# Performance work log

Measured on AMD Instinct MI355X. Metric: run time of the kernel, lower is better.

The kernel has to match this reference:

```python
import jax, jax.numpy as jnp
import numpy as np

DIM = 256
NUM_HEADS = 4
HEAD_DIM = DIM // NUM_HEADS
SCALE = HEAD_DIM ** -0.5


def setup_inputs() -> dict:
    key = jax.random.key(0)
    ks = jax.random.split(key, 6)
    B, S = 4, 4096
    x = jax.random.normal(ks[0], (B, S, DIM), dtype=jnp.float32)
    # nn.Linear weights are [out, in]; we store them that way and apply x @ W.T
    wq = jax.random.normal(ks[1], (DIM, DIM), dtype=jnp.float32) * (DIM ** -0.5)
    wk = jax.random.normal(ks[2], (DIM, DIM), dtype=jnp.float32) * (DIM ** -0.5)
    wv = jax.random.normal(ks[3], (DIM, DIM), dtype=jnp.float32) * (DIM ** -0.5)
    wo = jax.random.normal(ks[4], (DIM, DIM), dtype=jnp.float32) * (DIM ** -0.5)
    bo = jax.random.normal(ks[5], (DIM,), dtype=jnp.float32) * 0.02
    return {"x": x, "wq": wq, "wk": wk, "wv": wv, "wo": wo, "bo": bo}


def reference(x, wq, wk, wv, wo, bo):
    B, S, D = x.shape
    H, Hd = NUM_HEADS, HEAD_DIM
    # project and split heads: [B, H, S, Hd]
    q = (x @ wq.T).reshape(B, S, H, Hd).transpose(0, 2, 1, 3)
    k = (x @ wk.T).reshape(B, S, H, Hd).transpose(0, 2, 1, 3)
    v = (x @ wv.T).reshape(B, S, H, Hd).transpose(0, 2, 1, 3)
    attn = jnp.einsum('bhqd,bhkd->bhqk', q, k) * SCALE
    attn = jax.nn.softmax(attn, axis=-1)  # dropout is identity in eval mode
    out = jnp.einsum('bhqk,bhkd->bhqd', attn, v)
    out = out.transpose(0, 2, 1, 3).reshape(B, S, D)
    return out @ wo.T + bo
```

## Files before the change

### kernel.cpp

```cpp
#include <hip/hip_runtime.h>
#include <hip/hip_bf16.h>
#include <stdint.h>

#define DIM    256
#define NH     4
#define HD     64
#define BATCH  4
#define SEQ    4096
#define NTOK   (BATCH*SEQ)

typedef __bf16    bf16_t;
typedef _Float16  f16_t;
typedef _Float16  f16x8  __attribute__((ext_vector_type(8)));
typedef _Float16  f16x4  __attribute__((ext_vector_type(4)));
typedef float     f32x4  __attribute__((ext_vector_type(4)));
typedef float     f32x16 __attribute__((ext_vector_type(16)));
typedef unsigned short u16x8 __attribute__((ext_vector_type(8)));
typedef unsigned int   u32;
typedef u32 u32x2 __attribute__((ext_vector_type(2)));
typedef u32 u32x4 __attribute__((ext_vector_type(4)));

#define MFMA_F16    __builtin_amdgcn_mfma_f32_16x16x32_f16
#define MFMA32_F16  __builtin_amdgcn_mfma_f32_32x32x16_f16

#define QSCALE 0.18033688011112042f

#define WS_XA    ((size_t)0)
#define WS_Q     ((size_t)4194304)
#define WS_K     ((size_t)8388608)
#define WS_VT    ((size_t)12582912)
#define WS_W     ((size_t)16777216)
#define WS_BO    ((size_t)17039360)
#define WS_OATT  WS_XA

__device__ __forceinline__ size_t tiled_idx(int row, int k) {
  return ((size_t)(row >> 4) * 32 + (k >> 3)) * 128 + (row & 15) * 8 + (k & 7);
}

__device__ __forceinline__ void glds16(const void* g, void* l) {
  __builtin_amdgcn_global_load_lds(
      (const __attribute__((address_space(1))) void*)g,
      (__attribute__((address_space(3))) void*)l, 16, 0, 0);
}

__device__ __forceinline__ int detect_mode(const uint32_t* wq_u32) {
  uint32_t word = wq_u32[(threadIdx.x & 63) * 431 + 17];
  uint32_t b = (word >> 8) & 0x7fu;
  unsigned long long m = __ballot(b >= 0x38u && b <= 0x3fu);
  return (__popcll(m) >= 32) ? 0 : 1;
}

__device__ __forceinline__ f16x8 cvt_chunk(const void* src, size_t elem, int mode) {
  f16x8 r;
  if (mode) {
    const float* s = (const float*)src + elem;
    #pragma unroll
    for (int j = 0; j < 8; ++j) r[j] = (f16_t)s[j];
  } else {
    u16x8 v = *(const u16x8*)((const unsigned short*)src + elem);
    #pragma unroll
    for (int j = 0; j < 8; ++j) r[j] = (f16_t)__uint_as_float(((unsigned)v[j]) << 16);
  }
  return r;
}

__device__ __forceinline__ u32 pkh(float a, float b) {
  auto h = __builtin_amdgcn_cvt_pkrtz(a, b);
  return __builtin_bit_cast(u32, h);
}

__device__ __forceinline__ void swap32(u32& x, u32& y) {
#if __has_builtin(__builtin_amdgcn_permlane32_swap)
  u32x2 r = __builtin_amdgcn_permlane32_swap(x, y, false, false);
  x = r[0]; y = r[1];
#else
  u32 xp = __shfl_xor((int)x, 32), yp = __shfl_xor((int)y, 32);
  const bool h = (threadIdx.x & 32) != 0;
  u32 nx = h ? yp : x;
  u32 ny = h ? y  : xp;
  x = nx; y = ny;
#endif
}

__global__ __launch_bounds__(256) void cvt_all_kernel(
    const void* __restrict__ x,
    const void* __restrict__ wq, const void* __restrict__ wk,
    const void* __restrict__ wv, const void* __restrict__ wo,
    const void* __restrict__ bo,
    f16_t* __restrict__ xA, f16_t* __restrict__ wT,
    float* __restrict__ bof) {
  __shared__ int s_mode;
  if (threadIdx.x < 64) {
    int m = detect_mode((const uint32_t*)wq);
    if (threadIdx.x == 0) s_mode = m;
  }
  __syncthreads();
  const int mode = s_mode;
  const int bid = blockIdx.x;

  if (bid < 2048) {
    int idx = bid * 256 + (int)threadIdx.x;
    int tok = idx >> 5, kc = idx & 31;
    f16x8 r = cvt_chunk(x, (size_t)tok * DIM + kc * 8, mode);
    *(f16x8*)(xA + tiled_idx(tok, kc * 8)) = r;
  } else if (bid < 2176) {
    int idx = (bid - 2048) * 256 + (int)threadIdx.x;
    int which = idx >> 13, local = idx & 8191;
    const void* src = (which == 0) ? wq : (which == 1) ? wk : (which == 2) ? wv : wo;
    int n = local >> 5, kc = local & 31;
    f16x8 r = cvt_chunk(src, (size_t)n * DIM + kc * 8, mode);
    *(f16x8*)(wT + (size_t)which * 65536 + tiled_idx(n, kc * 8)) = r;
  } else {
    int i = threadIdx.x;
    bof[i] = mode ? ((const float*)bo)[i] : (float)((const bf16_t*)bo)[i];
  }
}

__global__ __launch_bounds__(256) void proj_fused_kernel(
    const f16_t* __restrict__ xA, const f16_t* __restrict__ wT,
    f16_t* __restrict__ q, f16_t* __restrict__ kk, f16_t* __restrict__ vt) {
  const int z    = blockIdx.z;
  const f16_t* w = wT + (size_t)z * 65536;
  const int lane = threadIdx.x & 63;
  const int wvi  = threadIdx.x >> 6;
  const int c    = lane & 15;
  const int g    = lane >> 4;

  if (z < 2) {
    const float scale = (z == 0) ? QSCALE : 1.0f;
    const int m0 = blockIdx.x * 64 + wvi * 16;
    const int n0 = blockIdx.y * 64;
    const f16_t* abase = xA + (size_t)(m0 >> 4) * 4096 + c * 8;
    const f16_t* bbase = w + (size_t)(n0 >> 4) * 4096 + c * 8;
    f32x4 acc[4] = {};
    #pragma unroll
    for (int ks = 0; ks < 8; ++ks) {
      const int kc = (ks * 4 + g) * 128;
      f16x8 a = *(const f16x8*)(abase + kc);
      #pragma unroll
      for (int nt = 0; nt < 4; ++nt) {
        f16x8 b = *(const f16x8*)(bbase + (size_t)nt * 4096 + kc);
        acc[nt] = MFMA_F16(a, b, acc[nt], 0, 0, 0);
      }
    }
    if (z == 0) {
      #pragma unroll
      for (int nt = 0; nt < 4; ++nt) {
        const int n = n0 + nt * 16 + c;
        const int h = n >> 6, d = n & 63;
        #pragma unroll
        for (int r = 0; r < 4; ++r) {
          const int tok = m0 + g * 4 + r;
          const int b = tok >> 12, s = tok & 4095;
          q[(size_t)((b * NH + h) * SEQ + s) * HD + d] = (f16_t)(acc[nt][r] * scale);
        }
      }
    } else {
      #pragma unroll
      for (int nt = 0; nt < 4; ++nt) {
        const int n = n0 + nt * 16 + c;
        const int h = n >> 6, d = n & 63;
        #pragma unroll
        for (int r = 0; r < 4; ++r) {
          const int tok = m0 + g * 4 + r;
          const int b = tok >> 12, s = tok & 4095;
          const int kt = s >> 6, row = s & 63;
          const int ch = (d >> 3) ^ (row & 7);
          kk[(size_t)(b * NH + h) * (SEQ * HD) + kt * 4096 + row * 64 + ch * 8 + (d & 7)]
              = (f16_t)acc[nt][r];
        }
      }
    }
  } else {
    const int m0 = blockIdx.y * 64 + wvi * 16;
    const int n0 = blockIdx.x * 64;
    const f16_t* abase = w + (size_t)(m0 >> 4) * 4096 + c * 8;
    const f16_t* bbase = xA + (size_t)(n0 >> 4) * 4096 + c * 8;
    f32x4 acc[4] = {};
    #pragma unroll
    for (int ks = 0; ks < 8; ++ks) {
      const int kc = (ks * 4 + g) * 128;
      f16x8 a = *(const f16x8*)(abase + kc);
      #pragma unroll
      for (int nt = 0; nt < 4; ++nt) {
        f16x8 b = *(const f16x8*)(bbase + (size_t)nt * 4096 + kc);
        acc[nt] = MFMA_F16(a, b, acc[nt], 0, 0, 0);
      }
    }
    #pragma unroll
    for (int nt = 0; nt < 4; ++nt) {
      const int tok = n0 + nt * 16 + c;
      const int b = tok >> 12, s = tok & 4095;
      const int kt = s >> 6, ko = s & 63;
      #pragma unroll
      for (int r = 0; r < 4; ++r) {
        const int vd = m0 + g * 4 + r;
        const int h = vd >> 6, d = vd & 63;
        const int ch = (ko >> 3) ^ (d & 7);
        vt[(size_t)(b * NH + h) * (SEQ * HD) + kt * 4096 + d * 64 + ch * 8 + (ko & 7)]
            = (f16_t)acc[nt][r];
      }
    }
  }
}

__global__ __launch_bounds__(256, 2) void attn_kernel(
    const f16_t* __restrict__ q, const f16_t* __restrict__ kimg,
    const f16_t* __restrict__ vimg, f16_t* __restrict__ o) {
  __shared__ __align__(16) f16_t smem[16896];

  const int tid = threadIdx.x;
  const int l   = tid & 63;
  const int w   = tid >> 6;
  const int wq_ = w & 1;
  const int wk_ = w >> 1;
  const int ql  = l & 31;
  const int hi  = l >> 5;
  const int bh  = blockIdx.x;
  const int q0  = blockIdx.y * 128;

  const f16_t* qb = q + ((size_t)bh * SEQ + q0 + wq_ * 64 + ql) * HD + hi * 8;
  f16x8 qf[2][4];
  #pragma unroll
  for (int qt = 0; qt < 2; ++qt)
    #pragma unroll
    for (int s = 0; s < 4; ++s)
      qf[qt][s] = *(const f16x8*)(qb + (size_t)qt * 32 * HD + s * 16);

  const char* kbase = (const char*)kimg + (size_t)bh * (SEQ * HD * 2);
  const char* vbase = (const char*)vimg + (size_t)bh * (SEQ * HD * 2);
  char* sB = (char*)smem;
  const int t16 = tid * 16;

  const int qx  = ql & 7;
  const int krow = wk_ * 32 + ql;
  int koff[4], voff[2][2];
  #pragma unroll
  for (int s = 0; s < 4; ++s)
    koff[s] = krow * 64 + (((s * 2 + hi) ^ qx) * 8);
  #pragma unroll
  for (int dt = 0; dt < 2; ++dt) {
    const int drow = dt * 32 + ql;
    #pragma unroll
    for (int kb = 0; kb < 2; ++kb)
      voff[dt][kb] = 4096 + drow * 64 + (((wk_ * 4 + kb * 2 + hi) ^ qx) * 8);
  }

  f32x16 acc[2][2] = {};
  float lsum[2] = {0.f, 0.f};

  glds16(kbase + t16,        sB + t16);
  glds16(kbase + 4096 + t16, sB + 4096 + t16);
  glds16(vbase + t16,        sB + 8192 + t16);
  glds16(vbase + 4096 + t16, sB + 12288 + t16);
  __syncthreads();

  for (int kt = 0; kt < SEQ / 64; ++kt) {
    const int bufo = (kt & 1) * 8192;
    const int bufB = (kt & 1) * 16384;
    if (kt < SEQ / 64 - 1) {
      const int nxtB = bufB ^ 16384;
      const size_t go = (size_t)(kt + 1) * 8192;
      glds16(kbase + go + t16,        sB + nxtB + t16);
      glds16(kbase + go + 4096 + t16, sB + nxtB + 4096 + t16);
      glds16(vbase + go + t16,        sB + nxtB + 8192 + t16);
      glds16(vbase + go + 4096 + t16, sB + nxtB + 12288 + t16);
    }

    f16x8 kf[4], vf[2][2];
    #pragma unroll
    for (int s = 0; s < 4; ++s)
      kf[s] = *(const f16x8*)(smem + bufo + koff[s]);
    #pragma unroll
    for (int dt = 0; dt < 2; ++dt)
      #pragma unroll
      for (int kb = 0; kb < 2; ++kb)
        vf[dt][kb] = *(const f16x8*)(smem + bufo + voff[dt][kb]);

    f16x8 pf[2][2];
    #pragma unroll
    for (int qt = 0; qt < 2; ++qt) {
      f32x16 st = {};
      #pragma unroll
      for (int s = 0; s < 4; ++s) st = MFMA32_F16(kf[s], qf[qt][s], st, 0, 0, 0);
      float p[16];
      #pragma unroll
      for (int r = 0; r < 16; ++r) p[r] = __builtin_amdgcn_exp2f(st[r]);
      float ls = 0.f;
      #pragma unroll
      for (int r = 0; r < 16; r += 4) ls += (p[r] + p[r + 1]) + (p[r + 2] + p[r + 3]);
      lsum[qt] += ls;
      #pragma unroll
      for (int kb = 0; kb < 2; ++kb) {
        u32 d0 = pkh(p[kb * 8 + 0], p[kb * 8 + 1]);
        u32 d1 = pkh(p[kb * 8 + 2], p[kb * 8 + 3]);
        u32 d2 = pkh(p[kb * 8 + 4], p[kb * 8 + 5]);
        u32 d3 = pkh(p[kb * 8 + 6], p[kb * 8 + 7]);
        swap32(d0, d2);
        swap32(d1, d3);
        u32x4 fd; fd[0] = d0; fd[1] = d1; fd[2] = d2; fd[3] = d3;
        pf[qt][kb] = __builtin_bit_cast(f16x8, fd);
      }
    }

    #pragma unroll
    for (int dt = 0; dt < 2; ++dt)
      #pragma unroll
      for (int qt = 0; qt < 2; ++qt) {
        f32x16 a = acc[dt][qt];
        a = MFMA32_F16(vf[dt][0], pf[qt][0], a, 0, 0, 0);
        a = MFMA32_F16(vf[dt][1], pf[qt][1], a, 0, 0, 0);
        acc[dt][qt] = a;
      }

    __syncthreads();
  }

  float* lred = (float*)(smem + 16384);
  #pragma unroll
  for (int qt = 0; qt < 2; ++qt) {
    lsum[qt] += __shfl_xor(lsum[qt], 32);
    if (hi == 0) lred[w * 64 + qt * 32 + ql] = lsum[qt];
  }
  float* red = (float*)smem;
  if (wk_ == 1) {
    #pragma unroll
    for (int t = 0; t < 4; ++t) {
      f32x16 a = acc[t >> 1][t & 1];
      #pragma unroll
      for (int qd = 0; qd < 4; ++qd) {
        f32x4 v = { a[qd * 4], a[qd * 4 + 1], a[qd * 4 + 2], a[qd * 4 + 3] };
        *(f32x4*)(red + wq_ * 4096 + (t * 4 + qd) * 256 + l * 4) = v;
      }
    }
  }
  __syncthreads();
  if (wk_ == 0) {
    float inv[2];
    #pragma unroll
    for (int qt = 0; qt < 2; ++qt)
      inv[qt] = 1.0f / (lred[w * 64 + qt * 32 + ql] + lred[(w + 2) * 64 + qt * 32 + ql]);

    const int b = bh >> 2, h = bh & 3;
    #pragma unroll
    for (int dt = 0; dt < 2; ++dt)
      #pragma unroll
      for (int qt = 0; qt < 2; ++qt) {
        const int t = dt * 2 + qt;
        f32x16 a = acc[dt][qt];
        const int tokg = b * SEQ + q0 + wq_ * 64 + qt * 32 + ql;
        const size_t rowbase = (size_t)(tokg >> 4) * 32 * 128 + (tokg & 15) * 8 + hi * 4;
        #pragma unroll
        for (int qd = 0; qd < 4; ++qd) {
          f32x4 v = *(const f32x4*)(red + wq_ * 4096 + (t * 4 + qd) * 256 + l * 4);
          f16x4 ov = { (f16_t)((a[qd * 4 + 0] + v[0]) * inv[qt]),
                       (f16_t)((a[qd * 4 + 1] + v[1]) * inv[qt]),
                       (f16_t)((a[qd * 4 + 2] + v[2]) * inv[qt]),
                       (f16_t)((a[qd * 4 + 3] + v[3]) * inv[qt]) };
          *(f16x4*)(o + rowbase + (size_t)(h * 8 + dt * 4 + qd) * 128) = ov;
        }
      }
  }
}

__global__ __launch_bounds__(256) void out_proj_kernel(
    const f16_t* __restrict__ aA, const f16_t* __restrict__ wT,
    const float* __restrict__ bo, void* __restrict__ outv,
    const void* __restrict__ wq_raw) {
  __shared__ int s_mode;
  if (threadIdx.x < 64) {
    int m = detect_mode((const uint32_t*)wq_raw);
    if (threadIdx.x == 0) s_mode = m;
  }
  __syncthreads();
  const int mode = s_mode;

  const int lane = threadIdx.x & 63;
  const int wv   = threadIdx.x >> 6;
  const int c    = lane & 15;
  const int g    = lane >> 4;
  const int m0   = blockIdx.x * 64 + wv * 16;
  const int n0   = blockIdx.y * 64;

  const f16_t* abase = aA + (size_t)(m0 >> 4) * 4096 + c * 8;
  const f16_t* bbase = wT + (size_t)(n0 >> 4) * 4096 + c * 8;
  f32x4 acc[4] = {};

  #pragma unroll
  for (int ks = 0; ks < 8; ++ks) {
    const int kc = (ks * 4 + g) * 128;
    f16x8 a = *(const f16x8*)(abase + kc);
    #pragma unroll
    for (int nt = 0; nt < 4; ++nt) {
      f16x8 b = *(const f16x8*)(bbase + (size_t)nt * 4096 + kc);
      acc[nt] = MFMA_F16(a, b, acc[nt], 0, 0, 0);
    }
  }

  #pragma unroll
  for (int nt = 0; nt < 4; ++nt) {
    const int n = n0 + nt * 16 + c;
    const float bias = bo[n];
    #pragma unroll
    for (int r = 0; r < 4; ++r) {
      const int tok = m0 + g * 4 + r;
      const float val = acc[nt][r] + bias;
      const size_t idx = (size_t)tok * DIM + n;
      if (mode) ((float*)outv)[idx] = val;
      else      ((bf16_t*)outv)[idx] = (bf16_t)val;
    }
  }
}

extern "C" void kernel_launch(void* const* d_in, const int* in_sizes, int n_in,
                              void* d_out, int out_size, void* d_ws, size_t ws_size,
                              hipStream_t stream) {
  (void)in_sizes; (void)n_in; (void)out_size; (void)ws_size;
  const void* x  = d_in[0];
  const void* wq = d_in[1];
  const void* wk = d_in[2];
  const void* wv = d_in[3];
  const void* wo = d_in[4];
  const void* bo = d_in[5];

  f16_t* ws    = (f16_t*)d_ws;
  f16_t* xA    = ws + WS_XA;
  f16_t* q     = ws + WS_Q;
  f16_t* kk    = ws + WS_K;
  f16_t* vt    = ws + WS_VT;
  f16_t* wT    = ws + WS_W;
  f16_t* woT   = ws + WS_W + 196608;
  float* bof   = (float*)(ws + WS_BO);
  f16_t* oattA = ws + WS_OATT;

  cvt_all_kernel   <<<dim3(2177),      256, 0, stream>>>(x, wq, wk, wv, wo, bo,
                                                         xA, wT, bof);
  proj_fused_kernel<<<dim3(256, 4, 3), 256, 0, stream>>>(xA, wT, q, kk, vt);
  attn_kernel      <<<dim3(16, 32),    256, 0, stream>>>(q, kk, vt, oattA);
  out_proj_kernel  <<<dim3(256, 4),    256, 0, stream>>>(oattA, woT, bof, d_out, wq);
}
```

Before: 183.6 us.

## Halve attention query tile to 64 rows, raise occupancy, add MFMA priority hints

The attention kernel now handles 64 query rows per block instead of 128, doubling the grid to 1024 blocks. Each wave keeps a single 32-row query tile, which reduces accumulator register pressure and allows launch bounds of 4 blocks per CU. MFMA sections are wrapped in s_setprio to favour matrix issue across waves. In exchange, each K/V tile loaded into shared memory is reused by half as many queries, so K/V traffic doubles.

```diff
diff --git a/kernel.cpp b/kernel.cpp
--- a/kernel.cpp
+++ b/kernel.cpp
@@ -204,10 +204,10 @@
   }
 }
 
-__global__ __launch_bounds__(256, 2) void attn_kernel(
+__global__ __launch_bounds__(256, 4) void attn_kernel(
     const f16_t* __restrict__ q, const f16_t* __restrict__ kimg,
     const f16_t* __restrict__ vimg, f16_t* __restrict__ o) {
-  __shared__ __align__(16) f16_t smem[16896];
+  __shared__ __align__(16) f16_t smem[16640];
 
   const int tid = threadIdx.x;
   const int l   = tid & 63;
@@ -217,15 +217,13 @@
   const int ql  = l & 31;
   const int hi  = l >> 5;
   const int bh  = blockIdx.x;
-  const int q0  = blockIdx.y * 128;
-
-  const f16_t* qb = q + ((size_t)bh * SEQ + q0 + wq_ * 64 + ql) * HD + hi * 8;
-  f16x8 qf[2][4];
+  const int q0  = blockIdx.y * 64;
+
+  const f16_t* qb = q + ((size_t)bh * SEQ + q0 + wq_ * 32 + ql) * HD + hi * 8;
+  f16x8 qf[4];
   #pragma unroll
-  for (int qt = 0; qt < 2; ++qt)
-    #pragma unroll
-    for (int s = 0; s < 4; ++s)
-      qf[qt][s] = *(const f16x8*)(qb + (size_t)qt * 32 * HD + s * 16);
+  for (int s = 0; s < 4; ++s)
+    qf[s] = *(const f16x8*)(qb + s * 16);
 
   const char* kbase = (const char*)kimg + (size_t)bh * (SEQ * HD * 2);
   const char* vbase = (const char*)vimg + (size_t)bh * (SEQ * HD * 2);
@@ -246,8 +244,8 @@
       voff[dt][kb] = 4096 + drow * 64 + (((wk_ * 4 + kb * 2 + hi) ^ qx) * 8);
   }
 
-  f32x16 acc[2][2] = {};
-  float lsum[2] = {0.f, 0.f};
+  f32x16 acc[2] = {};
+  float lsum = 0.f;
 
   glds16(kbase + t16,        sB + t16);
   glds16(kbase + 4096 + t16, sB + 4096 + t16);
@@ -277,89 +275,81 @@
       for (int kb = 0; kb < 2; ++kb)
         vf[dt][kb] = *(const f16x8*)(smem + bufo + voff[dt][kb]);
 
-    f16x8 pf[2][2];
-    #pragma unroll
-    for (int qt = 0; qt < 2; ++qt) {
-      f32x16 st = {};
-      #pragma unroll
-      for (int s = 0; s < 4; ++s) st = MFMA32_F16(kf[s], qf[qt][s], st, 0, 0, 0);
-      float p[16];
-      #pragma unroll
-      for (int r = 0; r < 16; ++r) p[r] = __builtin_amdgcn_exp2f(st[r]);
-      float ls = 0.f;
-      #pragma unroll
-      for (int r = 0; r < 16; r += 4) ls += (p[r] + p[r + 1]) + (p[r + 2] + p[r + 3]);
-      lsum[qt] += ls;
-      #pragma unroll
-      for (int kb = 0; kb < 2; ++kb) {
-        u32 d0 = pkh(p[kb * 8 + 0], p[kb * 8 + 1]);
-        u32 d1 = pkh(p[kb * 8 + 2], p[kb * 8 + 3]);
-        u32 d2 = pkh(p[kb * 8 + 4], p[kb * 8 + 5]);
-        u32 d3 = pkh(p[kb * 8 + 6], p[kb * 8 + 7]);
-        swap32(d0, d2);
-        swap32(d1, d3);
-        u32x4 fd; fd[0] = d0; fd[1] = d1; fd[2] = d2; fd[3] = d3;
-        pf[qt][kb] = __builtin_bit_cast(f16x8, fd);
-      }
-    }
-
-    #pragma unroll
-    for (int dt = 0; dt < 2; ++dt)
-      #pragma unroll
-      for (int qt = 0; qt < 2; ++qt) {
-        f32x16 a = acc[dt][qt];
-        a = MFMA32_F16(vf[dt][0], pf[qt][0], a, 0, 0, 0);
-        a = MFMA32_F16(vf[dt][1], pf[qt][1], a, 0, 0, 0);
-        acc[dt][qt] = a;
-      }
+    __builtin_amdgcn_s_setprio(1);
+    f32x16 st = {};
+    #pragma unroll
+    for (int s = 0; s < 4; ++s) st = MFMA32_F16(kf[s], qf[s], st, 0, 0, 0);
+    __builtin_amdgcn_s_setprio(0);
+
+    float p[16];
+    #pragma unroll
+    for (int r = 0; r < 16; ++r) p[r] = __builtin_amdgcn_exp2f(st[r]);
+    float ls = 0.f;
+    #pragma unroll
+    for (int r = 0; r < 16; r += 4) ls += (p[r] + p[r + 1]) + (p[r + 2] + p[r + 3]);
+    lsum += ls;
+    f16x8 pf[2];
+    #pragma unroll
+    for (int kb = 0; kb < 2; ++kb) {
+      u32 d0 = pkh(p[kb * 8 + 0], p[kb * 8 + 1]);
+      u32 d1 = pkh(p[kb * 8 + 2], p[kb * 8 + 3]);
+      u32 d2 = pkh(p[kb * 8 + 4], p[kb * 8 + 5]);
+      u32 d3 = pkh(p[kb * 8 + 6], p[kb * 8 + 7]);
+      swap32(d0, d2);
+      swap32(d1, d3);
+      u32x4 fd; fd[0] = d0; fd[1] = d1; fd[2] = d2; fd[3] = d3;
+      pf[kb] = __builtin_bit_cast(f16x8, fd);
+    }
+
+    __builtin_amdgcn_s_setprio(1);
+    #pragma unroll
+    for (int dt = 0; dt < 2; ++dt) {
+      f32x16 a = acc[dt];
+      a = MFMA32_F16(vf[dt][0], pf[0], a, 0, 0, 0);
+      a = MFMA32_F16(vf[dt][1], pf[1], a, 0, 0, 0);
+      acc[dt] = a;
+    }
+    __builtin_amdgcn_s_setprio(0);
 
     __syncthreads();
   }
 
   float* lred = (float*)(smem + 16384);
-  #pragma unroll
-  for (int qt = 0; qt < 2; ++qt) {
-    lsum[qt] += __shfl_xor(lsum[qt], 32);
-    if (hi == 0) lred[w * 64 + qt * 32 + ql] = lsum[qt];
-  }
+  lsum += __shfl_xor(lsum, 32);
+  if (hi == 0) lred[w * 32 + ql] = lsum;
+
   float* red = (float*)smem;
   if (wk_ == 1) {
     #pragma unroll
-    for (int t = 0; t < 4; ++t) {
-      f32x16 a = acc[t >> 1][t & 1];
+    for (int dt = 0; dt < 2; ++dt) {
+      f32x16 a = acc[dt];
       #pragma unroll
       for (int qd = 0; qd < 4; ++qd) {
         f32x4 v = { a[qd * 4], a[qd * 4 + 1], a[qd * 4 + 2], a[qd * 4 + 3] };
-        *(f32x4*)(red + wq_ * 4096 + (t * 4 + qd) * 256 + l * 4) = v;
+        *(f32x4*)(red + wq_ * 2048 + (dt * 4 + qd) * 256 + l * 4) = v;
       }
     }
   }
   __syncthreads();
   if (wk_ == 0) {
-    float inv[2];
-    #pragma unroll
-    for (int qt = 0; qt < 2; ++qt)
-      inv[qt] = 1.0f / (lred[w * 64 + qt * 32 + ql] + lred[(w + 2) * 64 + qt * 32 + ql]);
+    const float inv = 1.0f / (lred[w * 32 + ql] + lred[(w + 2) * 32 + ql]);
 
     const int b = bh >> 2, h = bh & 3;
-    #pragma unroll
-    for (int dt = 0; dt < 2; ++dt)
-      #pragma unroll
-      for (int qt = 0; qt < 2; ++qt) {
-        const int t = dt * 2 + qt;
-        f32x16 a = acc[dt][qt];
-        const int tokg = b * SEQ + q0 + wq_ * 64 + qt * 32 + ql;
-        const size_t rowbase = (size_t)(tokg >> 4) * 32 * 128 + (tokg & 15) * 8 + hi * 4;
-        #pragma unroll
-        for (int qd = 0; qd < 4; ++qd) {
-          f32x4 v = *(const f32x4*)(red + wq_ * 4096 + (t * 4 + qd) * 256 + l * 4);
-          f16x4 ov = { (f16_t)((a[qd * 4 + 0] + v[0]) * inv[qt]),
-                       (f16_t)((a[qd * 4 + 1] + v[1]) * inv[qt]),
-                       (f16_t)((a[qd * 4 + 2] + v[2]) * inv[qt]),
-                       (f16_t)((a[qd * 4 + 3] + v[3]) * inv[qt]) };
-          *(f16x4*)(o + rowbase + (size_t)(h * 8 + dt * 4 + qd) * 128) = ov;
-        }
-      }
+    const int tokg = b * SEQ + q0 + wq_ * 32 + ql;
+    const size_t rowbase = (size_t)(tokg >> 4) * 4096 + (tokg & 15) * 8 + hi * 4;
+    #pragma unroll
+    for (int dt = 0; dt < 2; ++dt) {
+      f32x16 a = acc[dt];
+      #pragma unroll
+      for (int qd = 0; qd < 4; ++qd) {
+        f32x4 v = *(const f32x4*)(red + wq_ * 2048 + (dt * 4 + qd) * 256 + l * 4);
+        f16x4 ov = { (f16_t)((a[qd * 4 + 0] + v[0]) * inv),
+                     (f16_t)((a[qd * 4 + 1] + v[1]) * inv),
+                     (f16_t)((a[qd * 4 + 2] + v[2]) * inv),
+                     (f16_t)((a[qd * 4 + 3] + v[3]) * inv) };
+        *(f16x4*)(o + rowbase + (size_t)(h * 8 + dt * 4 + qd) * 128) = ov;
+      }
+    }
   }
 }
 
@@ -436,6 +426,6 @@
   cvt_all_kernel   <<<dim3(2177),      256, 0, stream>>>(x, wq, wk, wv, wo, bo,
                                                          xA, wT, bof);
   proj_fused_kernel<<<dim3(256, 4, 3), 256, 0, stream>>>(xA, wT, q, kk, vt);
-  attn_kernel      <<<dim3(16, 32),    256, 0, stream>>>(q, kk, vt, oattA);
+  attn_kernel      <<<dim3(16, 64),    256, 0, stream>>>(q, kk, vt, oattA);
   out_proj_kernel  <<<dim3(256, 4),    256, 0, stream>>>(oattA, woT, bof, d_out, wq);
 }
```

Result: slower. 196.4 us (+7.0%).

## Split attention key loop across four waves per query tile with 128-key stages

Applied to the files above, without the earlier changes.

The attention kernel moves from 256 to 512 threads, so four waves share each 64-query group. Each wave handles one 32-key slice of a 128-key double-buffered stage, which halves the loop trip count and the number of barriers per key. Partial accumulators and row sums are merged through a two-step shared-memory reduction. s_setprio hints are placed around the MFMA sections. The cost is twice the LDS per block, heavier register pressure under launch_bounds(512,4), and a longer reduction epilogue.

```diff
diff --git a/kernel.cpp b/kernel.cpp
--- a/kernel.cpp
+++ b/kernel.cpp
@@ -204,16 +204,18 @@
   }
 }
 
-__global__ __launch_bounds__(256, 2) void attn_kernel(
+__global__ __launch_bounds__(512, 4) void attn_kernel(
     const f16_t* __restrict__ q, const f16_t* __restrict__ kimg,
     const f16_t* __restrict__ vimg, f16_t* __restrict__ o) {
-  __shared__ __align__(16) f16_t smem[16896];
+  __shared__ __align__(16) f16_t smem[33792];
 
   const int tid = threadIdx.x;
   const int l   = tid & 63;
   const int w   = tid >> 6;
-  const int wq_ = w & 1;
-  const int wk_ = w >> 1;
+  const int wq_ = w >> 2;
+  const int wk_ = w & 3;
+  const int su  = wk_ >> 1;
+  const int h2  = wk_ & 1;
   const int ql  = l & 31;
   const int hi  = l >> 5;
   const int bh  = blockIdx.x;
@@ -233,38 +235,38 @@
   const int t16 = tid * 16;
 
   const int qx  = ql & 7;
-  const int krow = wk_ * 32 + ql;
+  const int krow = h2 * 32 + ql;
   int koff[4], voff[2][2];
   #pragma unroll
   for (int s = 0; s < 4; ++s)
-    koff[s] = krow * 64 + (((s * 2 + hi) ^ qx) * 8);
+    koff[s] = su * 4096 + krow * 64 + (((s * 2 + hi) ^ qx) * 8);
   #pragma unroll
   for (int dt = 0; dt < 2; ++dt) {
     const int drow = dt * 32 + ql;
     #pragma unroll
     for (int kb = 0; kb < 2; ++kb)
-      voff[dt][kb] = 4096 + drow * 64 + (((wk_ * 4 + kb * 2 + hi) ^ qx) * 8);
+      voff[dt][kb] = 8192 + su * 4096 + drow * 64 + (((h2 * 4 + kb * 2 + hi) ^ qx) * 8);
   }
 
   f32x16 acc[2][2] = {};
   float lsum[2] = {0.f, 0.f};
 
-  glds16(kbase + t16,        sB + t16);
-  glds16(kbase + 4096 + t16, sB + 4096 + t16);
-  glds16(vbase + t16,        sB + 8192 + t16);
-  glds16(vbase + 4096 + t16, sB + 12288 + t16);
+  glds16(kbase + t16,         sB + t16);
+  glds16(kbase + 8192 + t16,  sB + 8192 + t16);
+  glds16(vbase + t16,         sB + 16384 + t16);
+  glds16(vbase + 8192 + t16,  sB + 24576 + t16);
   __syncthreads();
 
-  for (int kt = 0; kt < SEQ / 64; ++kt) {
-    const int bufo = (kt & 1) * 8192;
-    const int bufB = (kt & 1) * 16384;
-    if (kt < SEQ / 64 - 1) {
-      const int nxtB = bufB ^ 16384;
-      const size_t go = (size_t)(kt + 1) * 8192;
+  for (int kt = 0; kt < SEQ / 128; ++kt) {
+    const int bufo = (kt & 1) * 16384;
+    const int bufB = (kt & 1) * 32768;
+    if (kt < SEQ / 128 - 1) {
+      const int nxtB = bufB ^ 32768;
+      const size_t go = (size_t)(kt + 1) * 16384;
       glds16(kbase + go + t16,        sB + nxtB + t16);
-      glds16(kbase + go + 4096 + t16, sB + nxtB + 4096 + t16);
-      glds16(vbase + go + t16,        sB + nxtB + 8192 + t16);
-      glds16(vbase + go + 4096 + t16, sB + nxtB + 12288 + t16);
+      glds16(kbase + go + 8192 + t16, sB + nxtB + 8192 + t16);
+      glds16(vbase + go + t16,        sB + nxtB + 16384 + t16);
+      glds16(vbase + go + 8192 + t16, sB + nxtB + 24576 + t16);
     }
 
     f16x8 kf[4], vf[2][2];
@@ -280,9 +282,11 @@
     f16x8 pf[2][2];
     #pragma unroll
     for (int qt = 0; qt < 2; ++qt) {
+      __builtin_amdgcn_s_setprio(1);
       f32x16 st = {};
       #pragma unroll
       for (int s = 0; s < 4; ++s) st = MFMA32_F16(kf[s], qf[qt][s], st, 0, 0, 0);
+      __builtin_amdgcn_s_setprio(0);
       float p[16];
       #pragma unroll
       for (int r = 0; r < 16; ++r) p[r] = __builtin_amdgcn_exp2f(st[r]);
@@ -303,6 +307,7 @@
       }
     }
 
+    __builtin_amdgcn_s_setprio(1);
     #pragma unroll
     for (int dt = 0; dt < 2; ++dt)
       #pragma unroll
@@ -312,34 +317,68 @@
         a = MFMA32_F16(vf[dt][1], pf[qt][1], a, 0, 0, 0);
         acc[dt][qt] = a;
       }
+    __builtin_amdgcn_s_setprio(0);
 
     __syncthreads();
   }
 
-  float* lred = (float*)(smem + 16384);
+  float* lred = (float*)(smem + 32768);
   #pragma unroll
   for (int qt = 0; qt < 2; ++qt) {
     lsum[qt] += __shfl_xor(lsum[qt], 32);
     if (hi == 0) lred[w * 64 + qt * 32 + ql] = lsum[qt];
   }
   float* red = (float*)smem;
-  if (wk_ == 1) {
+  if (wk_ & 1) {
+    const int slot = wq_ * 2 + (wk_ >> 1);
     #pragma unroll
     for (int t = 0; t < 4; ++t) {
       f32x16 a = acc[t >> 1][t & 1];
       #pragma unroll
       for (int qd = 0; qd < 4; ++qd) {
         f32x4 v = { a[qd * 4], a[qd * 4 + 1], a[qd * 4 + 2], a[qd * 4 + 3] };
-        *(f32x4*)(red + wq_ * 4096 + (t * 4 + qd) * 256 + l * 4) = v;
+        *(f32x4*)(red + slot * 4096 + (t * 4 + qd) * 256 + l * 4) = v;
+      }
+    }
+  }
+  __syncthreads();
+  if (wk_ == 0 || wk_ == 2) {
+    const int slot = wq_ * 2 + (wk_ >> 1);
+    #pragma unroll
+    for (int t = 0; t < 4; ++t)
+      #pragma unroll
+      for (int qd = 0; qd < 4; ++qd) {
+        f32x4 v = *(const f32x4*)(red + slot * 4096 + (t * 4 + qd) * 256 + l * 4);
+        acc[t >> 1][t & 1][qd * 4 + 0] += v[0];
+        acc[t >> 1][t & 1][qd * 4 + 1] += v[1];
+        acc[t >> 1][t & 1][qd * 4 + 2] += v[2];
+        acc[t >> 1][t & 1][qd * 4 + 3] += v[3];
+      }
+  }
+  if (wk_ == 2) {
+    const int slot = wq_ * 2 + 1;
+    #pragma unroll
+    for (int t = 0; t < 4; ++t) {
+      f32x16 a = acc[t >> 1][t & 1];
+      #pragma unroll
+      for (int qd = 0; qd < 4; ++qd) {
+        f32x4 v = { a[qd * 4], a[qd * 4 + 1], a[qd * 4 + 2], a[qd * 4 + 3] };
+        *(f32x4*)(red + slot * 4096 + (t * 4 + qd) * 256 + l * 4) = v;
       }
     }
   }
   __syncthreads();
   if (wk_ == 0) {
+    const int slot = wq_ * 2 + 1;
     float inv[2];
     #pragma unroll
-    for (int qt = 0; qt < 2; ++qt)
-      inv[qt] = 1.0f / (lred[w * 64 + qt * 32 + ql] + lred[(w + 2) * 64 + qt * 32 + ql]);
+    for (int qt = 0; qt < 2; ++qt) {
+      float lt = 0.f;
+      #pragma unroll
+      for (int j = 0; j < 4; ++j)
+        lt += lred[(wq_ * 4 + j) * 64 + qt * 32 + ql];
+      inv[qt] = 1.0f / lt;
+    }
 
     const int b = bh >> 2, h = bh & 3;
     #pragma unroll
@@ -349,10 +388,10 @@
         const int t = dt * 2 + qt;
         f32x16 a = acc[dt][qt];
         const int tokg = b * SEQ + q0 + wq_ * 64 + qt * 32 + ql;
-        const size_t rowbase = (size_t)(tokg >> 4) * 32 * 128 + (tokg & 15) * 8 + hi * 4;
+        const size_t rowbase = (size_t)(tokg >> 4) * 4096 + (tokg & 15) * 8 + hi * 4;
         #pragma unroll
         for (int qd = 0; qd < 4; ++qd) {
-          f32x4 v = *(const f32x4*)(red + wq_ * 4096 + (t * 4 + qd) * 256 + l * 4);
+          f32x4 v = *(const f32x4*)(red + slot * 4096 + (t * 4 + qd) * 256 + l * 4);
           f16x4 ov = { (f16_t)((a[qd * 4 + 0] + v[0]) * inv[qt]),
                        (f16_t)((a[qd * 4 + 1] + v[1]) * inv[qt]),
                        (f16_t)((a[qd * 4 + 2] + v[2]) * inv[qt]),
@@ -436,6 +475,6 @@
   cvt_all_kernel   <<<dim3(2177),      256, 0, stream>>>(x, wq, wk, wv, wo, bo,
                                                          xA, wT, bof);
   proj_fused_kernel<<<dim3(256, 4, 3), 256, 0, stream>>>(xA, wT, q, kk, vt);
-  attn_kernel      <<<dim3(16, 32),    256, 0, stream>>>(q, kk, vt, oattA);
+  attn_kernel      <<<dim3(16, 32),    512, 0, stream>>>(q, kk, vt, oattA);
   out_proj_kernel  <<<dim3(256, 4),    256, 0, stream>>>(oattA, woT, bof, d_out, wq);
 }
```

New measurement: 607.5 us. +230.8%, slower.

## Software-pipeline attention loop so PV MFMAs of previous tile overlap current exp

Applied to the files above, without the earlier changes.

Restructures the attention inner loop into a software pipeline. The first K/V tile gets a prologue, the P·V MFMAs for tile kt-1 are issued right after the QK MFMAs for tile kt, and an epilogue drains the last tile. Wave priority is raised around the MFMA blocks with s_setprio so matrix work can overlap the exp2/pack VALU work of other waves. This costs extra registers for the carried V and P fragments, which may reduce occupancy.

```diff
diff --git a/kernel.cpp b/kernel.cpp
--- a/kernel.cpp
+++ b/kernel.cpp
@@ -248,6 +248,8 @@
 
   f32x16 acc[2][2] = {};
   float lsum[2] = {0.f, 0.f};
+  f16x8 vfp[2][2];
+  f16x8 pfp[2][2];
 
   glds16(kbase + t16,        sB + t16);
   glds16(kbase + 4096 + t16, sB + 4096 + t16);
@@ -255,7 +257,52 @@
   glds16(vbase + 4096 + t16, sB + 12288 + t16);
   __syncthreads();
 
-  for (int kt = 0; kt < SEQ / 64; ++kt) {
+  {
+    glds16(kbase + 8192 + t16,  sB + 16384 + t16);
+    glds16(kbase + 12288 + t16, sB + 20480 + t16);
+    glds16(vbase + 8192 + t16,  sB + 24576 + t16);
+    glds16(vbase + 12288 + t16, sB + 28672 + t16);
+
+    f16x8 kf[4];
+    #pragma unroll
+    for (int s = 0; s < 4; ++s)
+      kf[s] = *(const f16x8*)(smem + koff[s]);
+    #pragma unroll
+    for (int dt = 0; dt < 2; ++dt)
+      #pragma unroll
+      for (int kb = 0; kb < 2; ++kb)
+        vfp[dt][kb] = *(const f16x8*)(smem + voff[dt][kb]);
+
+    #pragma unroll
+    for (int qt = 0; qt < 2; ++qt) {
+      __builtin_amdgcn_s_setprio(1);
+      f32x16 st = {};
+      #pragma unroll
+      for (int s = 0; s < 4; ++s) st = MFMA32_F16(kf[s], qf[qt][s], st, 0, 0, 0);
+      __builtin_amdgcn_s_setprio(0);
+      float p[16];
+      #pragma unroll
+      for (int r = 0; r < 16; ++r) p[r] = __builtin_amdgcn_exp2f(st[r]);
+      float ls = 0.f;
+      #pragma unroll
+      for (int r = 0; r < 16; r += 4) ls += (p[r] + p[r + 1]) + (p[r + 2] + p[r + 3]);
+      lsum[qt] += ls;
+      #pragma unroll
+      for (int kb = 0; kb < 2; ++kb) {
+        u32 d0 = pkh(p[kb * 8 + 0], p[kb * 8 + 1]);
+        u32 d1 = pkh(p[kb * 8 + 2], p[kb * 8 + 3]);
+        u32 d2 = pkh(p[kb * 8 + 4], p[kb * 8 + 5]);
+        u32 d3 = pkh(p[kb * 8 + 6], p[kb * 8 + 7]);
+        swap32(d0, d2);
+        swap32(d1, d3);
+        u32x4 fd; fd[0] = d0; fd[1] = d1; fd[2] = d2; fd[3] = d3;
+        pfp[qt][kb] = __builtin_bit_cast(f16x8, fd);
+      }
+    }
+    __syncthreads();
+  }
+
+  for (int kt = 1; kt < SEQ / 64; ++kt) {
     const int bufo = (kt & 1) * 8192;
     const int bufB = (kt & 1) * 16384;
     if (kt < SEQ / 64 - 1) {
@@ -267,7 +314,7 @@
       glds16(vbase + go + 4096 + t16, sB + nxtB + 12288 + t16);
     }
 
-    f16x8 kf[4], vf[2][2];
+    f16x8 kf[4], vfc[2][2];
     #pragma unroll
     for (int s = 0; s < 4; ++s)
       kf[s] = *(const f16x8*)(smem + bufo + koff[s]);
@@ -275,17 +322,33 @@
     for (int dt = 0; dt < 2; ++dt)
       #pragma unroll
       for (int kb = 0; kb < 2; ++kb)
-        vf[dt][kb] = *(const f16x8*)(smem + bufo + voff[dt][kb]);
-
-    f16x8 pf[2][2];
+        vfc[dt][kb] = *(const f16x8*)(smem + bufo + voff[dt][kb]);
+
+    f32x16 st[2];
+    __builtin_amdgcn_s_setprio(1);
     #pragma unroll
     for (int qt = 0; qt < 2; ++qt) {
-      f32x16 st = {};
-      #pragma unroll
-      for (int s = 0; s < 4; ++s) st = MFMA32_F16(kf[s], qf[qt][s], st, 0, 0, 0);
+      f32x16 s0 = {};
+      #pragma unroll
+      for (int s = 0; s < 4; ++s) s0 = MFMA32_F16(kf[s], qf[qt][s], s0, 0, 0, 0);
+      st[qt] = s0;
+    }
+    #pragma unroll
+    for (int dt = 0; dt < 2; ++dt)
+      #pragma unroll
+      for (int qt = 0; qt < 2; ++qt) {
+        f32x16 a = acc[dt][qt];
+        a = MFMA32_F16(vfp[dt][0], pfp[qt][0], a, 0, 0, 0);
+        a = MFMA32_F16(vfp[dt][1], pfp[qt][1], a, 0, 0, 0);
+        acc[dt][qt] = a;
+      }
+    __builtin_amdgcn_s_setprio(0);
+
+    #pragma unroll
+    for (int qt = 0; qt < 2; ++qt) {
       float p[16];
       #pragma unroll
-      for (int r = 0; r < 16; ++r) p[r] = __builtin_amdgcn_exp2f(st[r]);
+      for (int r = 0; r < 16; ++r) p[r] = __builtin_amdgcn_exp2f(st[qt][r]);
       float ls = 0.f;
       #pragma unroll
       for (int r = 0; r < 16; r += 4) ls += (p[r] + p[r + 1]) + (p[r + 2] + p[r + 3]);
@@ -299,22 +362,29 @@
         swap32(d0, d2);
         swap32(d1, d3);
         u32x4 fd; fd[0] = d0; fd[1] = d1; fd[2] = d2; fd[3] = d3;
-        pf[qt][kb] = __builtin_bit_cast(f16x8, fd);
-      }
-    }
-
+        pfp[qt][kb] = __builtin_bit_cast(f16x8, fd);
+      }
+    }
     #pragma unroll
     for (int dt = 0; dt < 2; ++dt)
       #pragma unroll
-      for (int qt = 0; qt < 2; ++qt) {
-        f32x16 a = acc[dt][qt];
-        a = MFMA32_F16(vf[dt][0], pf[qt][0], a, 0, 0, 0);
-        a = MFMA32_F16(vf[dt][1], pf[qt][1], a, 0, 0, 0);
-        acc[dt][qt] = a;
-      }
+      for (int kb = 0; kb < 2; ++kb)
+        vfp[dt][kb] = vfc[dt][kb];
 
     __syncthreads();
   }
+
+  __builtin_amdgcn_s_setprio(1);
+  #pragma unroll
+  for (int dt = 0; dt < 2; ++dt)
+    #pragma unroll
+    for (int qt = 0; qt < 2; ++qt) {
+      f32x16 a = acc[dt][qt];
+      a = MFMA32_F16(vfp[dt][0], pfp[qt][0], a, 0, 0, 0);
+      a = MFMA32_F16(vfp[dt][1], pfp[qt][1], a, 0, 0, 0);
+      acc[dt][qt] = a;
+    }
+  __builtin_amdgcn_s_setprio(0);
 
   float* lred = (float*)(smem + 16384);
   #pragma unroll
@@ -349,7 +419,7 @@
         const int t = dt * 2 + qt;
         f32x16 a = acc[dt][qt];
         const int tokg = b * SEQ + q0 + wq_ * 64 + qt * 32 + ql;
-        const size_t rowbase = (size_t)(tokg >> 4) * 32 * 128 + (tokg & 15) * 8 + hi * 4;
+        const size_t rowbase = (size_t)(tokg >> 4) * 4096 + (tokg & 15) * 8 + hi * 4;
         #pragma unroll
         for (int qd = 0; qd < 4; ++qd) {
           f32x4 v = *(const f32x4*)(red + wq_ * 4096 + (t * 4 + qd) * 256 + l * 4);
```

Result: slower. 187.6 us (+2.2%).
